# Optimization experiments

Measured on AMD Instinct MI355X. Metric: run time of the kernel, lower is better.

The kernel has to match this reference:

```python
import jax, jax.numpy as jnp
import numpy as np

MAX_BITS = 64
HID = 768
B = 32768


def setup_inputs() -> dict:
    key = jax.random.key(0)
    ks = jax.random.split(key, 16)
    s = 0.02

    def w(k, shape):
        return jax.random.normal(k, shape, jnp.float32) * s

    a_bits = jnp.round(jax.random.uniform(ks[0], (B, MAX_BITS))).astype(jnp.float32)
    shift_amount = jax.random.randint(ks[1], (B,), 0, MAX_BITS).astype(jnp.int32)
    return {
        "a_bits": a_bits,
        "shift_amount": shift_amount,
        # shift_decoder: 64 -> 768 -> 768 -> 64 (weights stored [in, out])
        "Ws0": w(ks[2], (MAX_BITS, HID)), "bs0": jnp.zeros((HID,), jnp.float32),
        "Ws1": w(ks[3], (HID, HID)),      "bs1": jnp.zeros((HID,), jnp.float32),
        "Ws2": w(ks[4], (HID, MAX_BITS)), "bs2": jnp.zeros((MAX_BITS,), jnp.float32),
        # index_net: 128 -> 768 -> 768 -> 64
        "Wi0": w(ks[5], (2 * MAX_BITS, HID)), "bi0": jnp.zeros((HID,), jnp.float32),
        "Wi1": w(ks[6], (HID, HID)),          "bi1": jnp.zeros((HID,), jnp.float32),
        "Wi2": w(ks[7], (HID, MAX_BITS)),     "bi2": jnp.zeros((MAX_BITS,), jnp.float32),
        # validity_net: 128 -> 384 -> 1
        "Wv0": w(ks[8], (2 * MAX_BITS, HID // 2)), "bv0": jnp.zeros((HID // 2,), jnp.float32),
        "Wv1": w(ks[9], (HID // 2, 1)),            "bv1": jnp.zeros((1,), jnp.float32),
    }


def reference(a_bits, shift_amount, Ws0, bs0, Ws1, bs1, Ws2, bs2,
              Wi0, bi0, Wi1, bi1, Wi2, bi2, Wv0, bv0, Wv1, bv1):
    bits = a_bits.shape[1]  # == MAX_BITS == 64
    # decompose integer shift into bits: [B, bits]
    shift_bits = ((shift_amount[:, None] >> jnp.arange(bits, dtype=shift_amount.dtype)) & 1).astype(jnp.float32)
    # shift_decoder MLP -> hard one-hot of predicted shift
    h = jax.nn.relu(shift_bits @ Ws0 + bs0)
    h = jax.nn.relu(h @ Ws1 + bs1)
    shift_logits = (h @ Ws2 + bs2)[:, :bits]
    shift_soft = jax.nn.one_hot(jnp.argmax(shift_logits, axis=-1), bits, dtype=jnp.float32)  # [B, bits]
    # combined = [out_pos(one_hot(i)), shift_soft]; out_pos contribution to layer-0 is just row i of the
    # first `bits` rows of the weight, so precompute the shift_soft part once.
    base_i = shift_soft @ Wi0[bits:] + bi0   # [B, HID]
    base_v = shift_soft @ Wv0[bits:] + bv0   # [B, HID//2]

    def step(carry, i):
        h1 = jax.nn.relu(base_i + Wi0[i])                 # [B, HID]
        h2 = jax.nn.relu(h1 @ Wi1 + bi1)                  # [B, HID]
        idx_logits = (h2 @ Wi2 + bi2)[:, :bits]           # [B, bits]
        idx_soft = jax.nn.one_hot(jnp.argmax(idx_logits, axis=-1), bits, dtype=jnp.float32)
        pointed = jnp.sum(idx_soft * a_bits, axis=1)      # [B] soft gather
        hv = jax.nn.relu(base_v + Wv0[i])                 # [B, HID//2]
        valid = (hv @ Wv1 + bv1)[:, 0]                    # [B]
        return carry, pointed * jax.nn.sigmoid(valid)

    _, outs = jax.lax.scan(step, None, jnp.arange(bits))  # [bits, B]
    return outs.T                                          # [B, bits]
```

## Files before the change

### kernel.cpp

```cpp
#include <hip/hip_runtime.h>
#include <math.h>

#define HID 768
#define NB  64
#define HV  384

__device__ __forceinline__ float4 ld4(const float* p) { return *(const float4*)p; }

__global__ __launch_bounds__(256)
void dec1p_kernel(const float* __restrict__ Ws0, const float* __restrict__ bs0,
                  const float* __restrict__ Ws1, float* __restrict__ H1p) {
    __shared__ float W0s[7 * 48];
    __shared__ float As[48 * 68];
    __shared__ float Bs[48 * 68];
    const int tid = threadIdx.x;
    const int n0 = (blockIdx.x % 12) * 64;
    const int kz = blockIdx.x / 12;
    const int ks = kz * 48;

    for (int e = tid; e < 7 * 48; e += 256) {
        const int r = e / 48, c = e % 48;
        W0s[e] = (r < 6) ? Ws0[(size_t)r * HID + ks + c] : bs0[ks + c];
    }
    for (int e = tid; e < 48 * 16; e += 256) {
        const int k = e >> 4, nq = (e & 15) * 4;
        *(float4*)&Bs[k * 68 + nq] = ld4(Ws1 + (size_t)(ks + k) * HID + n0 + nq);
    }
    __syncthreads();
    for (int e = tid; e < 48 * 64; e += 256) {
        const int k = e >> 6, t = e & 63;
        float v = W0s[6 * 48 + k];
        #pragma unroll
        for (int b = 0; b < 6; ++b)
            v = fmaf((float)((t >> b) & 1), W0s[b * 48 + k], v);
        As[k * 68 + t] = fmaxf(v, 0.f);
    }
    __syncthreads();

    const int tx = tid & 15, ty = tid >> 4;
    float acc[4][4] = {};
    #pragma unroll 8
    for (int kk = 0; kk < 48; ++kk) {
        const float4 a4 = *(const float4*)&As[kk * 68 + ty * 4];
        const float4 b4 = *(const float4*)&Bs[kk * 68 + tx * 4];
        const float av[4] = {a4.x, a4.y, a4.z, a4.w};
        const float bv[4] = {b4.x, b4.y, b4.z, b4.w};
        #pragma unroll
        for (int a = 0; a < 4; ++a)
            #pragma unroll
            for (int b = 0; b < 4; ++b)
                acc[a][b] = fmaf(av[a], bv[b], acc[a][b]);
    }
    #pragma unroll
    for (int a = 0; a < 4; ++a) {
        float4 o = make_float4(acc[a][0], acc[a][1], acc[a][2], acc[a][3]);
        *(float4*)&H1p[((size_t)kz * 64 + ty * 4 + a) * HID + n0 + tx * 4] = o;
    }
}

__global__ __launch_bounds__(256)
void dec2_kernel(const float* __restrict__ H1p, const float* __restrict__ bs1,
                 const float* __restrict__ Ws2, const float* __restrict__ bs2,
                 int* __restrict__ pred) {
    __shared__ float sh[HID];
    __shared__ float plp[4][64];
    const int tid = threadIdx.x;
    const int t = blockIdx.x;

    for (int e = tid; e < HID / 4; e += 256) {
        const int k4 = e * 4;
        float4 v = ld4(bs1 + k4);
        #pragma unroll
        for (int z = 0; z < 16; ++z) {
            const float4 p = ld4(H1p + ((size_t)z * 64 + t) * HID + k4);
            v.x += p.x; v.y += p.y; v.z += p.z; v.w += p.w;
        }
        sh[k4 + 0] = fmaxf(v.x, 0.f);
        sh[k4 + 1] = fmaxf(v.y, 0.f);
        sh[k4 + 2] = fmaxf(v.z, 0.f);
        sh[k4 + 3] = fmaxf(v.w, 0.f);
    }
    __syncthreads();
    {
        const int n = tid & 63, part = tid >> 6;
        float p = 0.f;
        #pragma unroll 8
        for (int kk = 0; kk < 192; ++kk) {
            const int k = part * 192 + kk;
            p = fmaf(sh[k], Ws2[k * 64 + n], p);
        }
        plp[part][n] = p;
    }
    __syncthreads();
    if (tid == 0) {
        int best = 0;
        float bv = bs2[0] + plp[0][0] + plp[1][0] + plp[2][0] + plp[3][0];
        for (int n = 1; n < 64; ++n) {
            const float x = bs2[n] + plp[0][n] + plp[1][n] + plp[2][n] + plp[3][n];
            if (x > bv) { bv = x; best = n; }
        }
        pred[t] = best;
    }
}

__global__ __launch_bounds__(64)
void plan_kernel(const int* __restrict__ pred, int* __restrict__ hdr) {
    const int lane = threadIdx.x;
    __shared__ int present[64];
    present[lane] = 0;
    __syncthreads();
    present[pred[lane] & 63] = 1;
    __syncthreads();
    const unsigned long long alive = __ballot(present[lane] != 0);
    const int P = __popcll(alive);
    const int rank = __popcll(alive & ((1ull << lane) - 1ull));
    if (lane == 0) hdr[0] = P;
    if (present[lane]) { hdr[1 + rank] = lane; hdr[65 + lane] = rank; }
    else hdr[65 + lane] = -1;
}

__global__ __launch_bounds__(256)
void gemmA_kernel(const float* __restrict__ Wi0, const float* __restrict__ bi0,
                  const float* __restrict__ Wi1, const int* __restrict__ hdr,
                  float* __restrict__ H2p) {
    __shared__ float As[64 * 68];
    __shared__ float Bs[64 * 68];
    const int tid = threadIdx.x;
    const int P = hdr[0];
    const int li = blockIdx.y;
    if (li >= P) return;
    const int s = hdr[1 + li];
    const int n0 = blockIdx.x * 64;
    const int z = blockIdx.z;
    const int tx = tid & 15, ty = tid >> 4;
    const float* arow = Wi0 + (size_t)(64 + s) * HID;
    float acc[4][4] = {};

    for (int kt = 0; kt < 2; ++kt) {
        const int k0 = z * 128 + kt * 64;
        #pragma unroll
        for (int pass = 0; pass < 4; ++pass) {
            const int c = pass * 256 + tid;
            const int m = c >> 4, kq = (c & 15) * 4;
            const float4 a1 = ld4(arow + k0 + kq);
            const float4 a2 = ld4(Wi0 + (size_t)m * HID + k0 + kq);
            const float4 bb = ld4(bi0 + k0 + kq);
            As[(kq + 0) * 68 + m] = fmaxf(a1.x + a2.x + bb.x, 0.f);
            As[(kq + 1) * 68 + m] = fmaxf(a1.y + a2.y + bb.y, 0.f);
            As[(kq + 2) * 68 + m] = fmaxf(a1.z + a2.z + bb.z, 0.f);
            As[(kq + 3) * 68 + m] = fmaxf(a1.w + a2.w + bb.w, 0.f);
        }
        #pragma unroll
        for (int pass = 0; pass < 4; ++pass) {
            const int c = pass * 256 + tid;
            const int k = c >> 4, nq = (c & 15) * 4;
            *(float4*)&Bs[k * 68 + nq] = ld4(Wi1 + (size_t)(k0 + k) * HID + n0 + nq);
        }
        __syncthreads();
        #pragma unroll 8
        for (int kk = 0; kk < 64; ++kk) {
            const float4 a4 = *(const float4*)&As[kk * 68 + ty * 4];
            const float4 b4 = *(const float4*)&Bs[kk * 68 + tx * 4];
            const float av[4] = {a4.x, a4.y, a4.z, a4.w};
            const float bv[4] = {b4.x, b4.y, b4.z, b4.w};
            #pragma unroll
            for (int a = 0; a < 4; ++a)
                #pragma unroll
                for (int b = 0; b < 4; ++b)
                    acc[a][b] = fmaf(av[a], bv[b], acc[a][b]);
        }
        __syncthreads();
    }
    float* dst = H2p + ((size_t)(z * 64 + li) * 64) * HID + n0;
    #pragma unroll
    for (int a = 0; a < 4; ++a) {
        float4 o = make_float4(acc[a][0], acc[a][1], acc[a][2], acc[a][3]);
        *(float4*)(dst + (size_t)(ty * 4 + a) * HID + tx * 4) = o;
    }
}

__global__ __launch_bounds__(256)
void gemmB_kernel(const float* __restrict__ bi1, const float* __restrict__ Wi2,
                  const int* __restrict__ hdr, const float* __restrict__ H2p,
                  float* __restrict__ PLf) {
    __shared__ float Ht[64 * 68];
    __shared__ float W2[64 * 68];
    const int tid = threadIdx.x;
    const int P = hdr[0];
    const int li = blockIdx.y;
    if (li >= P) return;
    const int bx = blockIdx.x;
    const int n0 = bx * 64;
    const size_t zstep = (size_t)64 * 64 * HID;

    for (int e = tid; e < 1024; e += 256) {
        const int m = e >> 4, nq = (e & 15) * 4;
        const float* base = H2p + ((size_t)li * 64 + m) * HID + n0 + nq;
        float4 v = ld4(base);
        #pragma unroll
        for (int z = 1; z < 6; ++z) {
            const float4 p = ld4(base + z * zstep);
            v.x += p.x; v.y += p.y; v.z += p.z; v.w += p.w;
        }
        const float4 bb = ld4(bi1 + n0 + nq);
        Ht[(nq + 0) * 68 + m] = fmaxf(v.x + bb.x, 0.f);
        Ht[(nq + 1) * 68 + m] = fmaxf(v.y + bb.y, 0.f);
        Ht[(nq + 2) * 68 + m] = fmaxf(v.z + bb.z, 0.f);
        Ht[(nq + 3) * 68 + m] = fmaxf(v.w + bb.w, 0.f);
    }
    #pragma unroll
    for (int pass = 0; pass < 4; ++pass) {
        const int c = pass * 256 + tid;
        const int cl = c >> 4, oq = (c & 15) * 4;
        *(float4*)&W2[cl * 68 + oq] = ld4(Wi2 + (size_t)(n0 + cl) * 64 + oq);
    }
    __syncthreads();
    const int tx = tid & 15, ty = tid >> 4;
    float pl_[4][4] = {};
    #pragma unroll 16
    for (int kk = 0; kk < 64; ++kk) {
        const float4 a4 = *(const float4*)&Ht[kk * 68 + ty * 4];
        const float4 b4 = *(const float4*)&W2[kk * 68 + tx * 4];
        const float av[4] = {a4.x, a4.y, a4.z, a4.w};
        const float bv[4] = {b4.x, b4.y, b4.z, b4.w};
        #pragma unroll
        for (int a = 0; a < 4; ++a)
            #pragma unroll
            for (int b = 0; b < 4; ++b)
                pl_[a][b] = fmaf(av[a], bv[b], pl_[a][b]);
    }
    #pragma unroll
    for (int a = 0; a < 4; ++a) {
        float4 o = make_float4(pl_[a][0], pl_[a][1], pl_[a][2], pl_[a][3]);
        *(float4*)&PLf[((size_t)(bx * 64 + li) * 64 + ty * 4 + a) * 64 + tx * 4] = o;
    }
}

__global__ __launch_bounds__(256)
void reduceA_kernel(const float* __restrict__ PLf, const float* __restrict__ bi2,
                    const float* __restrict__ Wv0, const float* __restrict__ bv0,
                    const float* __restrict__ Wv1, const float* __restrict__ bv1,
                    const int* __restrict__ hdr,
                    int* __restrict__ j_tab, float* __restrict__ sig_tab) {
    __shared__ float lg[16 * 68];
    const int tid = threadIdx.x;
    const int s = blockIdx.x >> 2;
    const int li = hdr[65 + s];
    if (li < 0) return;
    const int r0 = blockIdx.x * 16;
    const int rr = tid >> 4, q = tid & 15;
    const int i = (r0 & 63) + rr;
    float4 v = ld4(bi2 + q * 4);
    #pragma unroll
    for (int bx = 0; bx < 12; ++bx) {
        const float4 p = ld4(PLf + ((size_t)(bx * 64 + li) * 64 + i) * 64 + q * 4);
        v.x += p.x; v.y += p.y; v.z += p.z; v.w += p.w;
    }
    *(float4*)&lg[rr * 68 + q * 4] = v;
    __syncthreads();
    if (tid < 16) {
        int best = 0; float bv = lg[tid * 68];
        for (int n = 1; n < 64; ++n) {
            const float x = lg[tid * 68 + n];
            if (x > bv) { bv = x; best = n; }
        }
        j_tab[r0 + tid] = best;
    }
    {
        const int r = r0 + rr;
        const int ii = r & 63;
        const float* w1 = Wv0 + (size_t)(64 + s) * HV;
        const float* w2 = Wv0 + (size_t)ii * HV;
        float sum = 0.f;
        #pragma unroll 4
        for (int c = q; c < HV; c += 16) {
            const float hv = fmaxf(w1[c] + w2[c] + bv0[c], 0.f);
            sum = fmaf(hv, Wv1[c], sum);
        }
        #pragma unroll
        for (int m = 8; m >= 1; m >>= 1) sum += __shfl_xor(sum, m);
        if (q == 0) sig_tab[r] = 1.f / (1.f + expf(-(sum + bv1[0])));
    }
}

__global__ __launch_bounds__(256)
void output_kernel(const float* __restrict__ a_bits, const int* __restrict__ shift_amount,
                   const int* __restrict__ pred, const int* __restrict__ j_tab,
                   const float* __restrict__ sig_tab, float* __restrict__ out, int B) {
    const int tid = threadIdx.x;
    const int i = tid & 63;
    const int b = blockIdx.x * 4 + (tid >> 6);
    if (b >= B) return;
    const int t = shift_amount[b] & 63;
    const int s = pred[t];
    const int idx = s * 64 + i;
    const int j = j_tab[idx];
    out[(size_t)b * 64 + i] = a_bits[(size_t)b * 64 + j] * sig_tab[idx];
}

extern "C" void kernel_launch(void* const* d_in, const int* in_sizes, int n_in,
                              void* d_out, int out_size, void* d_ws, size_t ws_size,
                              hipStream_t stream) {
    const float* a_bits       = (const float*)d_in[0];
    const int*   shift_amount = (const int*)d_in[1];
    const float* Ws0 = (const float*)d_in[2];
    const float* bs0 = (const float*)d_in[3];
    const float* Ws1 = (const float*)d_in[4];
    const float* bs1 = (const float*)d_in[5];
    const float* Ws2 = (const float*)d_in[6];
    const float* bs2 = (const float*)d_in[7];
    const float* Wi0 = (const float*)d_in[8];
    const float* bi0 = (const float*)d_in[9];
    const float* Wi1 = (const float*)d_in[10];
    const float* bi1 = (const float*)d_in[11];
    const float* Wi2 = (const float*)d_in[12];
    const float* bi2 = (const float*)d_in[13];
    const float* Wv0 = (const float*)d_in[14];
    const float* bv0 = (const float*)d_in[15];
    const float* Wv1 = (const float*)d_in[16];
    const float* bv1 = (const float*)d_in[17];
    float* out = (float*)d_out;
    const int B = in_sizes[1];

    char* ws = (char*)d_ws;
    int*   pred    = (int*)ws;
    int*   j_tab   = (int*)(ws + 1024);
    float* sig_tab = (float*)(ws + 20480);
    int*   hdr     = (int*)(ws + 40960);
    float* H1p = (float*)(ws + 65536);
    float* H2p = (float*)(ws + 65536);
    float* PLf = (float*)(ws + 65536 + 75497472);

    dec1p_kernel<<<192, 256, 0, stream>>>(Ws0, bs0, Ws1, H1p);
    dec2_kernel<<<64, 256, 0, stream>>>(H1p, bs1, Ws2, bs2, pred);
    plan_kernel<<<1, 64, 0, stream>>>(pred, hdr);
    gemmA_kernel<<<dim3(12, 64, 6), 256, 0, stream>>>(Wi0, bi0, Wi1, hdr, H2p);
    gemmB_kernel<<<dim3(12, 64), 256, 0, stream>>>(bi1, Wi2, hdr, H2p, PLf);
    reduceA_kernel<<<256, 256, 0, stream>>>(PLf, bi2, Wv0, bv0, Wv1, bv1, hdr,
                                            j_tab, sig_tab);
    output_kernel<<<(B + 3) / 4, 256, 0, stream>>>(a_bits, shift_amount, pred,
                                                   j_tab, sig_tab, out, B);
}
```

Measured before the change: 154.8 us.

## Fuse split-K index-net GEMMs into one kernel, dropping the H2 partial buffer

Merges the split-K first hidden GEMM (gemmA, grid z=6) and the second GEMM (gemmB) into one kernel. Each block now loops over all six K chunks itself, keeps the hidden tile in registers, applies bias and ReLU, and feeds it through shared memory into the Wi2 product. This removes the large H2p partial-sum buffer's global write and read, and one kernel launch. The cost is six times fewer blocks (12x64 instead of 12x64x6), each with a longer serial K loop, so parallelism across CUs drops, which matters when P (the number of distinct shifts) is small.

```diff
diff --git a/kernel.cpp b/kernel.cpp
--- a/kernel.cpp
+++ b/kernel.cpp
@@ -120,107 +120,89 @@
 }
 
 __global__ __launch_bounds__(256)
-void gemmA_kernel(const float* __restrict__ Wi0, const float* __restrict__ bi0,
-                  const float* __restrict__ Wi1, const int* __restrict__ hdr,
-                  float* __restrict__ H2p) {
-    __shared__ float As[64 * 68];
-    __shared__ float Bs[64 * 68];
+void gemmAB_kernel(const float* __restrict__ Wi0, const float* __restrict__ bi0,
+                   const float* __restrict__ Wi1, const float* __restrict__ bi1,
+                   const float* __restrict__ Wi2, const int* __restrict__ hdr,
+                   float* __restrict__ PLf) {
+    __shared__ float SA[64 * 68];
+    __shared__ float SB[64 * 68];
     const int tid = threadIdx.x;
     const int P = hdr[0];
     const int li = blockIdx.y;
     if (li >= P) return;
     const int s = hdr[1 + li];
-    const int n0 = blockIdx.x * 64;
-    const int z = blockIdx.z;
+    const int bx = blockIdx.x;
+    const int n0 = bx * 64;
     const int tx = tid & 15, ty = tid >> 4;
     const float* arow = Wi0 + (size_t)(64 + s) * HID;
-    float acc[4][4] = {};
-
-    for (int kt = 0; kt < 2; ++kt) {
-        const int k0 = z * 128 + kt * 64;
-        #pragma unroll
-        for (int pass = 0; pass < 4; ++pass) {
-            const int c = pass * 256 + tid;
-            const int m = c >> 4, kq = (c & 15) * 4;
-            const float4 a1 = ld4(arow + k0 + kq);
-            const float4 a2 = ld4(Wi0 + (size_t)m * HID + k0 + kq);
-            const float4 bb = ld4(bi0 + k0 + kq);
-            As[(kq + 0) * 68 + m] = fmaxf(a1.x + a2.x + bb.x, 0.f);
-            As[(kq + 1) * 68 + m] = fmaxf(a1.y + a2.y + bb.y, 0.f);
-            As[(kq + 2) * 68 + m] = fmaxf(a1.z + a2.z + bb.z, 0.f);
-            As[(kq + 3) * 68 + m] = fmaxf(a1.w + a2.w + bb.w, 0.f);
-        }
-        #pragma unroll
-        for (int pass = 0; pass < 4; ++pass) {
-            const int c = pass * 256 + tid;
-            const int k = c >> 4, nq = (c & 15) * 4;
-            *(float4*)&Bs[k * 68 + nq] = ld4(Wi1 + (size_t)(k0 + k) * HID + n0 + nq);
-        }
-        __syncthreads();
-        #pragma unroll 8
-        for (int kk = 0; kk < 64; ++kk) {
-            const float4 a4 = *(const float4*)&As[kk * 68 + ty * 4];
-            const float4 b4 = *(const float4*)&Bs[kk * 68 + tx * 4];
-            const float av[4] = {a4.x, a4.y, a4.z, a4.w};
-            const float bv[4] = {b4.x, b4.y, b4.z, b4.w};
-            #pragma unroll
-            for (int a = 0; a < 4; ++a)
+    float hs[4][4] = {};
+
+    for (int z = 0; z < 6; ++z) {
+        float acc[4][4] = {};
+        for (int kt = 0; kt < 2; ++kt) {
+            const int k0 = z * 128 + kt * 64;
+            #pragma unroll
+            for (int pass = 0; pass < 4; ++pass) {
+                const int c = pass * 256 + tid;
+                const int m = c >> 4, kq = (c & 15) * 4;
+                const float4 a1 = ld4(arow + k0 + kq);
+                const float4 a2 = ld4(Wi0 + (size_t)m * HID + k0 + kq);
+                const float4 bb = ld4(bi0 + k0 + kq);
+                SA[(kq + 0) * 68 + m] = fmaxf(a1.x + a2.x + bb.x, 0.f);
+                SA[(kq + 1) * 68 + m] = fmaxf(a1.y + a2.y + bb.y, 0.f);
+                SA[(kq + 2) * 68 + m] = fmaxf(a1.z + a2.z + bb.z, 0.f);
+                SA[(kq + 3) * 68 + m] = fmaxf(a1.w + a2.w + bb.w, 0.f);
+            }
+            #pragma unroll
+            for (int pass = 0; pass < 4; ++pass) {
+                const int c = pass * 256 + tid;
+                const int k = c >> 4, nq = (c & 15) * 4;
+                *(float4*)&SB[k * 68 + nq] = ld4(Wi1 + (size_t)(k0 + k) * HID + n0 + nq);
+            }
+            __syncthreads();
+            #pragma unroll 8
+            for (int kk = 0; kk < 64; ++kk) {
+                const float4 a4 = *(const float4*)&SA[kk * 68 + ty * 4];
+                const float4 b4 = *(const float4*)&SB[kk * 68 + tx * 4];
+                const float av[4] = {a4.x, a4.y, a4.z, a4.w};
+                const float bv[4] = {b4.x, b4.y, b4.z, b4.w};
                 #pragma unroll
-                for (int b = 0; b < 4; ++b)
-                    acc[a][b] = fmaf(av[a], bv[b], acc[a][b]);
-        }
-        __syncthreads();
-    }
-    float* dst = H2p + ((size_t)(z * 64 + li) * 64) * HID + n0;
-    #pragma unroll
-    for (int a = 0; a < 4; ++a) {
-        float4 o = make_float4(acc[a][0], acc[a][1], acc[a][2], acc[a][3]);
-        *(float4*)(dst + (size_t)(ty * 4 + a) * HID + tx * 4) = o;
-    }
-}
-
-__global__ __launch_bounds__(256)
-void gemmB_kernel(const float* __restrict__ bi1, const float* __restrict__ Wi2,
-                  const int* __restrict__ hdr, const float* __restrict__ H2p,
-                  float* __restrict__ PLf) {
-    __shared__ float Ht[64 * 68];
-    __shared__ float W2[64 * 68];
-    const int tid = threadIdx.x;
-    const int P = hdr[0];
-    const int li = blockIdx.y;
-    if (li >= P) return;
-    const int bx = blockIdx.x;
-    const int n0 = bx * 64;
-    const size_t zstep = (size_t)64 * 64 * HID;
-
-    for (int e = tid; e < 1024; e += 256) {
-        const int m = e >> 4, nq = (e & 15) * 4;
-        const float* base = H2p + ((size_t)li * 64 + m) * HID + n0 + nq;
-        float4 v = ld4(base);
-        #pragma unroll
-        for (int z = 1; z < 6; ++z) {
-            const float4 p = ld4(base + z * zstep);
-            v.x += p.x; v.y += p.y; v.z += p.z; v.w += p.w;
-        }
-        const float4 bb = ld4(bi1 + n0 + nq);
-        Ht[(nq + 0) * 68 + m] = fmaxf(v.x + bb.x, 0.f);
-        Ht[(nq + 1) * 68 + m] = fmaxf(v.y + bb.y, 0.f);
-        Ht[(nq + 2) * 68 + m] = fmaxf(v.z + bb.z, 0.f);
-        Ht[(nq + 3) * 68 + m] = fmaxf(v.w + bb.w, 0.f);
+                for (int a = 0; a < 4; ++a)
+                    #pragma unroll
+                    for (int b = 0; b < 4; ++b)
+                        acc[a][b] = fmaf(av[a], bv[b], acc[a][b]);
+            }
+            __syncthreads();
+        }
+        #pragma unroll
+        for (int a = 0; a < 4; ++a)
+            #pragma unroll
+            for (int b = 0; b < 4; ++b)
+                hs[a][b] += acc[a][b];
+    }
+
+    {
+        const float4 bb = ld4(bi1 + n0 + tx * 4);
+        const float bbv[4] = {bb.x, bb.y, bb.z, bb.w};
+        #pragma unroll
+        for (int a = 0; a < 4; ++a)
+            #pragma unroll
+            for (int b = 0; b < 4; ++b)
+                SA[(tx * 4 + b) * 68 + ty * 4 + a] = fmaxf(hs[a][b] + bbv[b], 0.f);
     }
     #pragma unroll
     for (int pass = 0; pass < 4; ++pass) {
         const int c = pass * 256 + tid;
         const int cl = c >> 4, oq = (c & 15) * 4;
-        *(float4*)&W2[cl * 68 + oq] = ld4(Wi2 + (size_t)(n0 + cl) * 64 + oq);
-    }
-    __syncthreads();
-    const int tx = tid & 15, ty = tid >> 4;
+        *(float4*)&SB[cl * 68 + oq] = ld4(Wi2 + (size_t)(n0 + cl) * 64 + oq);
+    }
+    __syncthreads();
+
     float pl_[4][4] = {};
     #pragma unroll 16
     for (int kk = 0; kk < 64; ++kk) {
-        const float4 a4 = *(const float4*)&Ht[kk * 68 + ty * 4];
-        const float4 b4 = *(const float4*)&W2[kk * 68 + tx * 4];
+        const float4 a4 = *(const float4*)&SA[kk * 68 + ty * 4];
+        const float4 b4 = *(const float4*)&SB[kk * 68 + tx * 4];
         const float av[4] = {a4.x, a4.y, a4.z, a4.w};
         const float bv[4] = {b4.x, b4.y, b4.z, b4.w};
         #pragma unroll
@@ -328,14 +310,12 @@
     float* sig_tab = (float*)(ws + 20480);
     int*   hdr     = (int*)(ws + 40960);
     float* H1p = (float*)(ws + 65536);
-    float* H2p = (float*)(ws + 65536);
     float* PLf = (float*)(ws + 65536 + 75497472);
 
     dec1p_kernel<<<192, 256, 0, stream>>>(Ws0, bs0, Ws1, H1p);
     dec2_kernel<<<64, 256, 0, stream>>>(H1p, bs1, Ws2, bs2, pred);
     plan_kernel<<<1, 64, 0, stream>>>(pred, hdr);
-    gemmA_kernel<<<dim3(12, 64, 6), 256, 0, stream>>>(Wi0, bi0, Wi1, hdr, H2p);
-    gemmB_kernel<<<dim3(12, 64), 256, 0, stream>>>(bi1, Wi2, hdr, H2p, PLf);
+    gemmAB_kernel<<<dim3(12, 64), 256, 0, stream>>>(Wi0, bi0, Wi1, bi1, Wi2, hdr, PLf);
     reduceA_kernel<<<256, 256, 0, stream>>>(PLf, bi2, Wv0, bv0, Wv1, bv1, hdr,
                                             j_tab, sig_tab);
     output_kernel<<<(B + 3) / 4, 256, 0, stream>>>(a_bits, shift_amount, pred,
```

Measured after the change: 182.0 us. +17.5%, slower.
